# Kernel optimization log

Measured on AMD Instinct MI355X. Metric: run time of the kernel, lower is better.

The kernel has to match this reference:

```python
import jax, jax.numpy as jnp
import numpy as np
from jax import lax

B, C, H, W = 32, 256, 56, 56
K = 3  # kernel_size

def setup_inputs() -> dict:
    key = jax.random.key(0)
    k1, k2, k3 = jax.random.split(key, 3)
    x = jax.random.normal(k1, (B, C, H, W), dtype=jnp.float32)
    # 1x1 conv weight Conv2d(C, C*K*K, 1) flattened to a linear map [C*K*K, C]
    Wk = jax.random.normal(k2, (C * K * K, C), dtype=jnp.float32) * 0.02
    bk = jax.random.normal(k3, (C * K * K,), dtype=jnp.float32) * 0.02
    return {"x": x, "Wk": Wk, "bk": bk}

def reference(x, Wk, bk):
    b, c, h, w = x.shape
    # kernel generator: global avg pool -> 1x1 conv -> relu
    pooled = x.mean(axis=(2, 3))                       # [B, C]
    kern = jax.nn.relu(pooled @ Wk.T + bk)             # [B, C*K*K]
    kern = kern.reshape(b * c, 1, K, K)                # OIHW, one filter per (b,c)
    # per-sample, per-channel depthwise conv: groups = B*C
    xr = x.reshape(1, b * c, h, w)
    out = lax.conv_general_dilated(
        xr, kern,
        window_strides=(1, 1),
        padding=[(K // 2, K // 2), (K // 2, K // 2)],
        feature_group_count=b * c,
        dimension_numbers=("NCHW", "OIHW", "NCHW"),
    )
    return out.reshape(b, c, h, w)
```

## Files before the change

kernel.cpp:

```cpp
#include <hip/hip_runtime.h>

#define B_  32
#define C_  256
#define H_  56
#define W_  56
#define HW  3136
#define KK  9
#define OC  2304
#define NPLANES (B_*C_)

typedef float v4f __attribute__((ext_vector_type(4)));

__global__ __launch_bounds__(256) void pool_kernel(const float* __restrict__ x,
                                                   float* __restrict__ pooled) {
    const int wid  = threadIdx.x >> 6;
    const int lane = threadIdx.x & 63;
    const int plane = blockIdx.x * 4 + wid;
    const float4* xp = (const float4*)(x + (size_t)plane * HW);

    float s = 0.f;
    #pragma unroll
    for (int k = 0; k < 12; ++k) {
        float4 v = xp[lane + k * 64];
        s += (v.x + v.y) + (v.z + v.w);
    }
    if (lane < 16) {
        float4 v = xp[768 + lane];
        s += (v.x + v.y) + (v.z + v.w);
    }
    #pragma unroll
    for (int off = 32; off > 0; off >>= 1)
        s += __shfl_down(s, off, 64);
    if (lane == 0)
        pooled[plane] = s * (1.0f / (float)HW);
}

__global__ __launch_bounds__(256) void dconv_kernel(const float* __restrict__ x,
                                                    const float* __restrict__ pooled,
                                                    const float* __restrict__ Wk,
                                                    const float* __restrict__ bk,
                                                    float* __restrict__ out) {
    const int plane = blockIdx.x;
    const int b = plane >> 8;
    const int c = plane & 255;
    __shared__ float lds[58 * 58];
    __shared__ float wsh[KK];
    const int t = threadIdx.x;

    const float4* xp = (const float4*)(x + (size_t)plane * HW);
    float4 v0 = xp[t];
    float4 v1 = xp[t + 256];
    float4 v2 = xp[t + 512];
    float4 v3 = make_float4(0.f, 0.f, 0.f, 0.f);
    if (t < 16) v3 = xp[t + 768];

    if (t < 144) {
        const int o  = t >> 4;
        const int ch = (t & 15) << 4;
        const int og = c * KK + o;
        const float4* wr = (const float4*)(Wk + (size_t)og * C_ + ch);
        const float4* pr = (const float4*)(pooled + b * C_ + ch);
        float s = 0.f;
        #pragma unroll
        for (int i = 0; i < 4; ++i) {
            float4 w = wr[i];
            float4 p = pr[i];
            s += w.x * p.x + w.y * p.y + w.z * p.z + w.w * p.w;
        }
        #pragma unroll
        for (int off = 8; off > 0; off >>= 1)
            s += __shfl_down(s, off, 16);
        if ((t & 15) == 0)
            wsh[o] = fmaxf(s + bk[og], 0.f);
    }

    if (t < 58) { lds[t] = 0.f; lds[57 * 58 + t] = 0.f; }
    if (t < 56) { lds[(t + 1) * 58] = 0.f; lds[(t + 1) * 58 + 57] = 0.f; }

    {
        int s, r, c0, base;
        s = t;        r = s / 14; c0 = (s % 14) * 4; base = (r + 1) * 58 + c0 + 1;
        lds[base] = v0.x; lds[base + 1] = v0.y; lds[base + 2] = v0.z; lds[base + 3] = v0.w;
        s = t + 256;  r = s / 14; c0 = (s % 14) * 4; base = (r + 1) * 58 + c0 + 1;
        lds[base] = v1.x; lds[base + 1] = v1.y; lds[base + 2] = v1.z; lds[base + 3] = v1.w;
        s = t + 512;  r = s / 14; c0 = (s % 14) * 4; base = (r + 1) * 58 + c0 + 1;
        lds[base] = v2.x; lds[base + 1] = v2.y; lds[base + 2] = v2.z; lds[base + 3] = v2.w;
        if (t < 16) {
            s = t + 768; r = s / 14; c0 = (s % 14) * 4; base = (r + 1) * 58 + c0 + 1;
            lds[base] = v3.x; lds[base + 1] = v3.y; lds[base + 2] = v3.z; lds[base + 3] = v3.w;
        }
    }

    __syncthreads();

    const float w0 = wsh[0], w1 = wsh[1], w2 = wsh[2],
                w3 = wsh[3], w4 = wsh[4], w5 = wsh[5],
                w6 = wsh[6], w7 = wsh[7], w8 = wsh[8];

    float* op = out + (size_t)plane * HW;

    for (int i = t; i < 392; i += 256) {
        const int rp = i / 14;
        const int c0 = (i % 14) * 4;
        const float* R0 = &lds[(2 * rp + 0) * 58 + c0];
        const float* R1 = &lds[(2 * rp + 1) * 58 + c0];
        const float* R2 = &lds[(2 * rp + 2) * 58 + c0];
        const float* R3 = &lds[(2 * rp + 3) * 58 + c0];
        float2 p0 = *(const float2*)(R0), p1 = *(const float2*)(R0 + 2), p2 = *(const float2*)(R0 + 4);
        float2 q0 = *(const float2*)(R1), q1 = *(const float2*)(R1 + 2), q2 = *(const float2*)(R1 + 4);
        float2 r0 = *(const float2*)(R2), r1 = *(const float2*)(R2 + 2), r2 = *(const float2*)(R2 + 4);
        float2 s0 = *(const float2*)(R3), s1 = *(const float2*)(R3 + 2), s2 = *(const float2*)(R3 + 4);
        const float a0 = p0.x, a1 = p0.y, a2 = p1.x, a3 = p1.y, a4 = p2.x, a5 = p2.y;
        const float b0 = q0.x, b1 = q0.y, b2 = q1.x, b3 = q1.y, b4 = q2.x, b5 = q2.y;
        const float c0f = r0.x, c1f = r0.y, c2f = r1.x, c3f = r1.y, c4f = r2.x, c5f = r2.y;
        const float d0 = s0.x, d1 = s0.y, d2 = s1.x, d3 = s1.y, d4 = s2.x, d5 = s2.y;

        v4f t0, t1;
        t0.x = a0*w0 + a1*w1 + a2*w2 + b0*w3 + b1*w4 + b2*w5 + c0f*w6 + c1f*w7 + c2f*w8;
        t0.y = a1*w0 + a2*w1 + a3*w2 + b1*w3 + b2*w4 + b3*w5 + c1f*w6 + c2f*w7 + c3f*w8;
        t0.z = a2*w0 + a3*w1 + a4*w2 + b2*w3 + b3*w4 + b4*w5 + c2f*w6 + c3f*w7 + c4f*w8;
        t0.w = a3*w0 + a4*w1 + a5*w2 + b3*w3 + b4*w4 + b5*w5 + c3f*w6 + c4f*w7 + c5f*w8;
        t1.x = b0*w0 + b1*w1 + b2*w2 + c0f*w3 + c1f*w4 + c2f*w5 + d0*w6 + d1*w7 + d2*w8;
        t1.y = b1*w0 + b2*w1 + b3*w2 + c1f*w3 + c2f*w4 + c3f*w5 + d1*w6 + d2*w7 + d3*w8;
        t1.z = b2*w0 + b3*w1 + b4*w2 + c2f*w3 + c3f*w4 + c4f*w5 + d2*w6 + d3*w7 + d4*w8;
        t1.w = b3*w0 + b4*w1 + b5*w2 + c3f*w3 + c4f*w4 + c5f*w5 + d3*w6 + d4*w7 + d5*w8;

        __builtin_nontemporal_store(t0, (v4f*)(op + (2 * rp + 0) * W_ + c0));
        __builtin_nontemporal_store(t1, (v4f*)(op + (2 * rp + 1) * W_ + c0));
    }
}

extern "C" void kernel_launch(void* const* d_in, const int* in_sizes, int n_in,
                              void* d_out, int out_size, void* d_ws, size_t ws_size,
                              hipStream_t stream) {
    const float* x  = (const float*)d_in[0];
    const float* Wk = (const float*)d_in[1];
    const float* bk = (const float*)d_in[2];
    float* out = (float*)d_out;

    float* pooled = (float*)d_ws;

    pool_kernel<<<NPLANES / 4, 256, 0, stream>>>(x, pooled);
    dconv_kernel<<<NPLANES, 256, 0, stream>>>(x, pooled, Wk, bk, out);
}
```

Measured before the change: 198.9 us.

## Process eight planes per block with double-buffered LDS staging and coalesced stores

The depthwise conv kernel becomes persistent-style: each block walks eight consecutive planes. While it computes the current plane, it prefetches the next plane and its generated filter into registers and a second LDS buffer. Output is staged through an LDS tile, so global stores are fully contiguous float4 writes. This aims to hide global load latency and cut per-block launch overhead, but it uses much more LDS per block (about 39KB) and adds an extra barrier per plane, which lowers occupancy and parallelism (1024 blocks instead of 8192).

```diff
diff --git a/kernel.cpp b/kernel.cpp
--- a/kernel.cpp
+++ b/kernel.cpp
@@ -6,8 +6,9 @@
 #define W_  56
 #define HW  3136
 #define KK  9
-#define OC  2304
 #define NPLANES (B_*C_)
+#define NP  8
+#define DGRID (NPLANES/NP)
 
 typedef float v4f __attribute__((ext_vector_type(4)));
 
@@ -35,26 +36,14 @@
         pooled[plane] = s * (1.0f / (float)HW);
 }
 
-__global__ __launch_bounds__(256) void dconv_kernel(const float* __restrict__ x,
-                                                    const float* __restrict__ pooled,
-                                                    const float* __restrict__ Wk,
-                                                    const float* __restrict__ bk,
-                                                    float* __restrict__ out) {
-    const int plane = blockIdx.x;
-    const int b = plane >> 8;
-    const int c = plane & 255;
-    __shared__ float lds[58 * 58];
-    __shared__ float wsh[KK];
-    const int t = threadIdx.x;
-
-    const float4* xp = (const float4*)(x + (size_t)plane * HW);
-    float4 v0 = xp[t];
-    float4 v1 = xp[t + 256];
-    float4 v2 = xp[t + 512];
-    float4 v3 = make_float4(0.f, 0.f, 0.f, 0.f);
-    if (t < 16) v3 = xp[t + 768];
-
+__device__ __forceinline__ void kerngen(int t, int plane,
+                                        const float* __restrict__ pooled,
+                                        const float* __restrict__ Wk,
+                                        const float* __restrict__ bk,
+                                        float* __restrict__ wdst) {
     if (t < 144) {
+        const int b  = plane >> 8;
+        const int c  = plane & 255;
         const int o  = t >> 4;
         const int ch = (t & 15) << 4;
         const int og = c * KK + o;
@@ -71,62 +60,115 @@
         for (int off = 8; off > 0; off >>= 1)
             s += __shfl_down(s, off, 16);
         if ((t & 15) == 0)
-            wsh[o] = fmaxf(s + bk[og], 0.f);
+            wdst[o] = fmaxf(s + bk[og], 0.f);
+    }
+}
+
+__device__ __forceinline__ void stage_write(float* __restrict__ dst, int t,
+                                            float4 v0, float4 v1, float4 v2, float4 v3) {
+    int s, r, c0, base;
+    s = t;        r = s / 14; c0 = (s % 14) * 4; base = (r + 1) * 58 + c0 + 1;
+    dst[base] = v0.x; dst[base + 1] = v0.y; dst[base + 2] = v0.z; dst[base + 3] = v0.w;
+    s = t + 256;  r = s / 14; c0 = (s % 14) * 4; base = (r + 1) * 58 + c0 + 1;
+    dst[base] = v1.x; dst[base + 1] = v1.y; dst[base + 2] = v1.z; dst[base + 3] = v1.w;
+    s = t + 512;  r = s / 14; c0 = (s % 14) * 4; base = (r + 1) * 58 + c0 + 1;
+    dst[base] = v2.x; dst[base + 1] = v2.y; dst[base + 2] = v2.z; dst[base + 3] = v2.w;
+    if (t < 16) {
+        s = t + 768; r = s / 14; c0 = (s % 14) * 4; base = (r + 1) * 58 + c0 + 1;
+        dst[base] = v3.x; dst[base + 1] = v3.y; dst[base + 2] = v3.z; dst[base + 3] = v3.w;
+    }
+}
+
+__global__ __launch_bounds__(256, 4) void dconv_kernel(const float* __restrict__ x,
+                                                       const float* __restrict__ pooled,
+                                                       const float* __restrict__ Wk,
+                                                       const float* __restrict__ bk,
+                                                       float* __restrict__ out) {
+    __shared__ float buf[2][58 * 58];
+    __shared__ float ost[56 * 56];
+    __shared__ float wsh[2][16];
+
+    const int t  = threadIdx.x;
+    const int p0 = blockIdx.x * NP;
+
+    #pragma unroll
+    for (int q = 0; q < 2; ++q) {
+        if (t < 58) { buf[q][t] = 0.f; buf[q][57 * 58 + t] = 0.f; }
+        if (t < 56) { buf[q][(t + 1) * 58] = 0.f; buf[q][(t + 1) * 58 + 57] = 0.f; }
     }
 
-    if (t < 58) { lds[t] = 0.f; lds[57 * 58 + t] = 0.f; }
-    if (t < 56) { lds[(t + 1) * 58] = 0.f; lds[(t + 1) * 58 + 57] = 0.f; }
-
+    float4 s0, s1, s2, s3 = make_float4(0.f, 0.f, 0.f, 0.f);
     {
-        int s, r, c0, base;
-        s = t;        r = s / 14; c0 = (s % 14) * 4; base = (r + 1) * 58 + c0 + 1;
-        lds[base] = v0.x; lds[base + 1] = v0.y; lds[base + 2] = v0.z; lds[base + 3] = v0.w;
-        s = t + 256;  r = s / 14; c0 = (s % 14) * 4; base = (r + 1) * 58 + c0 + 1;
-        lds[base] = v1.x; lds[base + 1] = v1.y; lds[base + 2] = v1.z; lds[base + 3] = v1.w;
-        s = t + 512;  r = s / 14; c0 = (s % 14) * 4; base = (r + 1) * 58 + c0 + 1;
-        lds[base] = v2.x; lds[base + 1] = v2.y; lds[base + 2] = v2.z; lds[base + 3] = v2.w;
-        if (t < 16) {
-            s = t + 768; r = s / 14; c0 = (s % 14) * 4; base = (r + 1) * 58 + c0 + 1;
-            lds[base] = v3.x; lds[base + 1] = v3.y; lds[base + 2] = v3.z; lds[base + 3] = v3.w;
-        }
+        const float4* xp = (const float4*)(x + (size_t)p0 * HW);
+        s0 = xp[t]; s1 = xp[t + 256]; s2 = xp[t + 512];
+        if (t < 16) s3 = xp[t + 768];
     }
-
+    kerngen(t, p0, pooled, Wk, bk, wsh[0]);
+    stage_write(buf[0], t, s0, s1, s2, s3);
     __syncthreads();
 
-    const float w0 = wsh[0], w1 = wsh[1], w2 = wsh[2],
-                w3 = wsh[3], w4 = wsh[4], w5 = wsh[5],
-                w6 = wsh[6], w7 = wsh[7], w8 = wsh[8];
+    for (int p = 0; p < NP; ++p) {
+        const int cur = p & 1, nxt = cur ^ 1;
+        const bool more = (p + 1 < NP);
 
-    float* op = out + (size_t)plane * HW;
+        if (more) {
+            const float4* xp = (const float4*)(x + (size_t)(p0 + p + 1) * HW);
+            s0 = xp[t]; s1 = xp[t + 256]; s2 = xp[t + 512];
+            if (t < 16) s3 = xp[t + 768];
+            kerngen(t, p0 + p + 1, pooled, Wk, bk, wsh[nxt]);
+        }
 
-    for (int i = t; i < 392; i += 256) {
-        const int rp = i / 14;
-        const int c0 = (i % 14) * 4;
-        const float* R0 = &lds[(2 * rp + 0) * 58 + c0];
-        const float* R1 = &lds[(2 * rp + 1) * 58 + c0];
-        const float* R2 = &lds[(2 * rp + 2) * 58 + c0];
-        const float* R3 = &lds[(2 * rp + 3) * 58 + c0];
-        float2 p0 = *(const float2*)(R0), p1 = *(const float2*)(R0 + 2), p2 = *(const float2*)(R0 + 4);
-        float2 q0 = *(const float2*)(R1), q1 = *(const float2*)(R1 + 2), q2 = *(const float2*)(R1 + 4);
-        float2 r0 = *(const float2*)(R2), r1 = *(const float2*)(R2 + 2), r2 = *(const float2*)(R2 + 4);
-        float2 s0 = *(const float2*)(R3), s1 = *(const float2*)(R3 + 2), s2 = *(const float2*)(R3 + 4);
-        const float a0 = p0.x, a1 = p0.y, a2 = p1.x, a3 = p1.y, a4 = p2.x, a5 = p2.y;
-        const float b0 = q0.x, b1 = q0.y, b2 = q1.x, b3 = q1.y, b4 = q2.x, b5 = q2.y;
-        const float c0f = r0.x, c1f = r0.y, c2f = r1.x, c3f = r1.y, c4f = r2.x, c5f = r2.y;
-        const float d0 = s0.x, d1 = s0.y, d2 = s1.x, d3 = s1.y, d4 = s2.x, d5 = s2.y;
+        {
+            const float* wc = wsh[cur];
+            const float w0 = wc[0], w1 = wc[1], w2 = wc[2],
+                        w3 = wc[3], w4 = wc[4], w5 = wc[5],
+                        w6 = wc[6], w7 = wc[7], w8 = wc[8];
+            const float* bs = buf[cur];
+            for (int i = t; i < 392; i += 256) {
+                const int rp = i / 14;
+                const int c0 = (i % 14) * 4;
+                const float* R0 = &bs[(2 * rp + 0) * 58 + c0];
+                const float* R1 = &bs[(2 * rp + 1) * 58 + c0];
+                const float* R2 = &bs[(2 * rp + 2) * 58 + c0];
+                const float* R3 = &bs[(2 * rp + 3) * 58 + c0];
+                float2 p0v = *(const float2*)(R0), p1v = *(const float2*)(R0 + 2), p2v = *(const float2*)(R0 + 4);
+                float2 q0v = *(const float2*)(R1), q1v = *(const float2*)(R1 + 2), q2v = *(const float2*)(R1 + 4);
+                float2 r0v = *(const float2*)(R2), r1v = *(const float2*)(R2 + 2), r2v = *(const float2*)(R2 + 4);
+                float2 u0v = *(const float2*)(R3), u1v = *(const float2*)(R3 + 2), u2v = *(const float2*)(R3 + 4);
+                const float a0 = p0v.x, a1 = p0v.y, a2 = p1v.x, a3 = p1v.y, a4 = p2v.x, a5 = p2v.y;
+                const float b0 = q0v.x, b1 = q0v.y, b2 = q1v.x, b3 = q1v.y, b4 = q2v.x, b5 = q2v.y;
+                const float e0 = r0v.x, e1 = r0v.y, e2 = r1v.x, e3 = r1v.y, e4 = r2v.x, e5 = r2v.y;
+                const float d0 = u0v.x, d1 = u0v.y, d2 = u1v.x, d3 = u1v.y, d4 = u2v.x, d5 = u2v.y;
 
-        v4f t0, t1;
-        t0.x = a0*w0 + a1*w1 + a2*w2 + b0*w3 + b1*w4 + b2*w5 + c0f*w6 + c1f*w7 + c2f*w8;
-        t0.y = a1*w0 + a2*w1 + a3*w2 + b1*w3 + b2*w4 + b3*w5 + c1f*w6 + c2f*w7 + c3f*w8;
-        t0.z = a2*w0 + a3*w1 + a4*w2 + b2*w3 + b3*w4 + b4*w5 + c2f*w6 + c3f*w7 + c4f*w8;
-        t0.w = a3*w0 + a4*w1 + a5*w2 + b3*w3 + b4*w4 + b5*w5 + c3f*w6 + c4f*w7 + c5f*w8;
-        t1.x = b0*w0 + b1*w1 + b2*w2 + c0f*w3 + c1f*w4 + c2f*w5 + d0*w6 + d1*w7 + d2*w8;
-        t1.y = b1*w0 + b2*w1 + b3*w2 + c1f*w3 + c2f*w4 + c3f*w5 + d1*w6 + d2*w7 + d3*w8;
-        t1.z = b2*w0 + b3*w1 + b4*w2 + c2f*w3 + c3f*w4 + c4f*w5 + d2*w6 + d3*w7 + d4*w8;
-        t1.w = b3*w0 + b4*w1 + b5*w2 + c3f*w3 + c4f*w4 + c5f*w5 + d3*w6 + d4*w7 + d5*w8;
+                v4f t0, t1;
+                t0.x = a0*w0 + a1*w1 + a2*w2 + b0*w3 + b1*w4 + b2*w5 + e0*w6 + e1*w7 + e2*w8;
+                t0.y = a1*w0 + a2*w1 + a3*w2 + b1*w3 + b2*w4 + b3*w5 + e1*w6 + e2*w7 + e3*w8;
+                t0.z = a2*w0 + a3*w1 + a4*w2 + b2*w3 + b3*w4 + b4*w5 + e2*w6 + e3*w7 + e4*w8;
+                t0.w = a3*w0 + a4*w1 + a5*w2 + b3*w3 + b4*w4 + b5*w5 + e3*w6 + e4*w7 + e5*w8;
+                t1.x = b0*w0 + b1*w1 + b2*w2 + e0*w3 + e1*w4 + e2*w5 + d0*w6 + d1*w7 + d2*w8;
+                t1.y = b1*w0 + b2*w1 + b3*w2 + e1*w3 + e2*w4 + e3*w5 + d1*w6 + d2*w7 + d3*w8;
+                t1.z = b2*w0 + b3*w1 + b4*w2 + e2*w3 + e3*w4 + e4*w5 + d2*w6 + d3*w7 + d4*w8;
+                t1.w = b3*w0 + b4*w1 + b5*w2 + e3*w3 + e4*w4 + e5*w5 + d3*w6 + d4*w7 + d5*w8;
 
-        __builtin_nontemporal_store(t0, (v4f*)(op + (2 * rp + 0) * W_ + c0));
-        __builtin_nontemporal_store(t1, (v4f*)(op + (2 * rp + 1) * W_ + c0));
+                *(v4f*)&ost[(2 * rp + 0) * 56 + c0] = t0;
+                *(v4f*)&ost[(2 * rp + 1) * 56 + c0] = t1;
+            }
+        }
+        __syncthreads();
+
+        {
+            float* op = out + (size_t)(p0 + p) * HW;
+            const v4f* os = (const v4f*)ost;
+            __builtin_nontemporal_store(os[t],       (v4f*)op + t);
+            __builtin_nontemporal_store(os[t + 256], (v4f*)op + t + 256);
+            __builtin_nontemporal_store(os[t + 512], (v4f*)op + t + 512);
+            if (t < 16)
+                __builtin_nontemporal_store(os[t + 768], (v4f*)op + t + 768);
+        }
+
+        if (more)
+            stage_write(buf[nxt], t, s0, s1, s2, s3);
+        __syncthreads();
     }
 }
 
@@ -141,5 +183,5 @@
     float* pooled = (float*)d_ws;
 
     pool_kernel<<<NPLANES / 4, 256, 0, stream>>>(x, pooled);
-    dconv_kernel<<<NPLANES, 256, 0, stream>>>(x, pooled, Wk, bk, out);
+    dconv_kernel<<<DGRID, 256, 0, stream>>>(x, pooled, Wk, bk, out);
 }
```

Measured after the change: 206.4 us. 3.8% more time.

## Drop LDS halo tile in depthwise conv, read neighbours directly from global/cache

Applied to the files above, without the earlier changes.

The padded 58x58 shared-memory tile and its staging stores are removed. Each thread now loads its four input rows straight from global memory, using float4 loads plus scalar left and right halo loads, and handles the zero padding with predicates. Launch bounds add a minimum-blocks hint of 8 to raise occupancy now that LDS use is minimal. The trade is more redundant global and L1/L2 traffic from overlapping halo reads and unaligned scalar loads, in exchange for removing the LDS round trip.

```diff
diff --git a/kernel.cpp b/kernel.cpp
--- a/kernel.cpp
+++ b/kernel.cpp
@@ -6,7 +6,6 @@
 #define W_  56
 #define HW  3136
 #define KK  9
-#define OC  2304
 #define NPLANES (B_*C_)
 
 typedef float v4f __attribute__((ext_vector_type(4)));
@@ -35,24 +34,16 @@
         pooled[plane] = s * (1.0f / (float)HW);
 }
 
-__global__ __launch_bounds__(256) void dconv_kernel(const float* __restrict__ x,
-                                                    const float* __restrict__ pooled,
-                                                    const float* __restrict__ Wk,
-                                                    const float* __restrict__ bk,
-                                                    float* __restrict__ out) {
+__global__ __launch_bounds__(256, 8) void dconv_kernel(const float* __restrict__ x,
+                                                       const float* __restrict__ pooled,
+                                                       const float* __restrict__ Wk,
+                                                       const float* __restrict__ bk,
+                                                       float* __restrict__ out) {
     const int plane = blockIdx.x;
     const int b = plane >> 8;
     const int c = plane & 255;
-    __shared__ float lds[58 * 58];
     __shared__ float wsh[KK];
     const int t = threadIdx.x;
-
-    const float4* xp = (const float4*)(x + (size_t)plane * HW);
-    float4 v0 = xp[t];
-    float4 v1 = xp[t + 256];
-    float4 v2 = xp[t + 512];
-    float4 v3 = make_float4(0.f, 0.f, 0.f, 0.f);
-    if (t < 16) v3 = xp[t + 768];
 
     if (t < 144) {
         const int o  = t >> 4;
@@ -73,58 +64,80 @@
         if ((t & 15) == 0)
             wsh[o] = fmaxf(s + bk[og], 0.f);
     }
-
-    if (t < 58) { lds[t] = 0.f; lds[57 * 58 + t] = 0.f; }
-    if (t < 56) { lds[(t + 1) * 58] = 0.f; lds[(t + 1) * 58 + 57] = 0.f; }
-
-    {
-        int s, r, c0, base;
-        s = t;        r = s / 14; c0 = (s % 14) * 4; base = (r + 1) * 58 + c0 + 1;
-        lds[base] = v0.x; lds[base + 1] = v0.y; lds[base + 2] = v0.z; lds[base + 3] = v0.w;
-        s = t + 256;  r = s / 14; c0 = (s % 14) * 4; base = (r + 1) * 58 + c0 + 1;
-        lds[base] = v1.x; lds[base + 1] = v1.y; lds[base + 2] = v1.z; lds[base + 3] = v1.w;
-        s = t + 512;  r = s / 14; c0 = (s % 14) * 4; base = (r + 1) * 58 + c0 + 1;
-        lds[base] = v2.x; lds[base + 1] = v2.y; lds[base + 2] = v2.z; lds[base + 3] = v2.w;
-        if (t < 16) {
-            s = t + 768; r = s / 14; c0 = (s % 14) * 4; base = (r + 1) * 58 + c0 + 1;
-            lds[base] = v3.x; lds[base + 1] = v3.y; lds[base + 2] = v3.z; lds[base + 3] = v3.w;
-        }
-    }
-
     __syncthreads();
 
     const float w0 = wsh[0], w1 = wsh[1], w2 = wsh[2],
                 w3 = wsh[3], w4 = wsh[4], w5 = wsh[5],
                 w6 = wsh[6], w7 = wsh[7], w8 = wsh[8];
 
+    const float* xp = x + (size_t)plane * HW;
     float* op = out + (size_t)plane * HW;
 
     for (int i = t; i < 392; i += 256) {
         const int rp = i / 14;
         const int c0 = (i % 14) * 4;
-        const float* R0 = &lds[(2 * rp + 0) * 58 + c0];
-        const float* R1 = &lds[(2 * rp + 1) * 58 + c0];
-        const float* R2 = &lds[(2 * rp + 2) * 58 + c0];
-        const float* R3 = &lds[(2 * rp + 3) * 58 + c0];
-        float2 p0 = *(const float2*)(R0), p1 = *(const float2*)(R0 + 2), p2 = *(const float2*)(R0 + 4);
-        float2 q0 = *(const float2*)(R1), q1 = *(const float2*)(R1 + 2), q2 = *(const float2*)(R1 + 4);
-        float2 r0 = *(const float2*)(R2), r1 = *(const float2*)(R2 + 2), r2 = *(const float2*)(R2 + 4);
-        float2 s0 = *(const float2*)(R3), s1 = *(const float2*)(R3 + 2), s2 = *(const float2*)(R3 + 4);
-        const float a0 = p0.x, a1 = p0.y, a2 = p1.x, a3 = p1.y, a4 = p2.x, a5 = p2.y;
-        const float b0 = q0.x, b1 = q0.y, b2 = q1.x, b3 = q1.y, b4 = q2.x, b5 = q2.y;
-        const float c0f = r0.x, c1f = r0.y, c2f = r1.x, c3f = r1.y, c4f = r2.x, c5f = r2.y;
-        const float d0 = s0.x, d1 = s0.y, d2 = s1.x, d3 = s1.y, d4 = s2.x, d5 = s2.y;
+        const bool cl = (c0 > 0);
+        const bool cr = (c0 < 52);
+
+        float a00 = 0.f, a01 = 0.f, a02 = 0.f, a03 = 0.f;
+        float a10 = 0.f, a11 = 0.f, a12 = 0.f, a13 = 0.f;
+
+        {
+            const int r = 2 * rp - 1;
+            const float* rw = xp + (r < 0 ? 0 : r) * W_;
+            float4 m = *(const float4*)(rw + c0);
+            float vl = cl ? rw[c0 - 1] : 0.f;
+            float vr = cr ? rw[c0 + 4] : 0.f;
+            if (r < 0) { m.x = 0.f; m.y = 0.f; m.z = 0.f; m.w = 0.f; vl = 0.f; vr = 0.f; }
+            a00 += w0 * vl  + w1 * m.x + w2 * m.y;
+            a01 += w0 * m.x + w1 * m.y + w2 * m.z;
+            a02 += w0 * m.y + w1 * m.z + w2 * m.w;
+            a03 += w0 * m.z + w1 * m.w + w2 * vr;
+        }
+        {
+            const float* rw = xp + (2 * rp) * W_;
+            float4 m = *(const float4*)(rw + c0);
+            float vl = cl ? rw[c0 - 1] : 0.f;
+            float vr = cr ? rw[c0 + 4] : 0.f;
+            a00 += w3 * vl  + w4 * m.x + w5 * m.y;
+            a01 += w3 * m.x + w4 * m.y + w5 * m.z;
+            a02 += w3 * m.y + w4 * m.z + w5 * m.w;
+            a03 += w3 * m.z + w4 * m.w + w5 * vr;
+            a10 += w0 * vl  + w1 * m.x + w2 * m.y;
+            a11 += w0 * m.x + w1 * m.y + w2 * m.z;
+            a12 += w0 * m.y + w1 * m.z + w2 * m.w;
+            a13 += w0 * m.z + w1 * m.w + w2 * vr;
+        }
+        {
+            const float* rw = xp + (2 * rp + 1) * W_;
+            float4 m = *(const float4*)(rw + c0);
+            float vl = cl ? rw[c0 - 1] : 0.f;
+            float vr = cr ? rw[c0 + 4] : 0.f;
+            a00 += w6 * vl  + w7 * m.x + w8 * m.y;
+            a01 += w6 * m.x + w7 * m.y + w8 * m.z;
+            a02 += w6 * m.y + w7 * m.z + w8 * m.w;
+            a03 += w6 * m.z + w7 * m.w + w8 * vr;
+            a10 += w3 * vl  + w4 * m.x + w5 * m.y;
+            a11 += w3 * m.x + w4 * m.y + w5 * m.z;
+            a12 += w3 * m.y + w4 * m.z + w5 * m.w;
+            a13 += w3 * m.z + w4 * m.w + w5 * vr;
+        }
+        {
+            const int r = 2 * rp + 2;
+            const float* rw = xp + (r > 55 ? 55 : r) * W_;
+            float4 m = *(const float4*)(rw + c0);
+            float vl = cl ? rw[c0 - 1] : 0.f;
+            float vr = cr ? rw[c0 + 4] : 0.f;
+            if (r > 55) { m.x = 0.f; m.y = 0.f; m.z = 0.f; m.w = 0.f; vl = 0.f; vr = 0.f; }
+            a10 += w6 * vl  + w7 * m.x + w8 * m.y;
+            a11 += w6 * m.x + w7 * m.y + w8 * m.z;
+            a12 += w6 * m.y + w7 * m.z + w8 * m.w;
+            a13 += w6 * m.z + w7 * m.w + w8 * vr;
+        }
 
         v4f t0, t1;
-        t0.x = a0*w0 + a1*w1 + a2*w2 + b0*w3 + b1*w4 + b2*w5 + c0f*w6 + c1f*w7 + c2f*w8;
-        t0.y = a1*w0 + a2*w1 + a3*w2 + b1*w3 + b2*w4 + b3*w5 + c1f*w6 + c2f*w7 + c3f*w8;
-        t0.z = a2*w0 + a3*w1 + a4*w2 + b2*w3 + b3*w4 + b4*w5 + c2f*w6 + c3f*w7 + c4f*w8;
-        t0.w = a3*w0 + a4*w1 + a5*w2 + b3*w3 + b4*w4 + b5*w5 + c3f*w6 + c4f*w7 + c5f*w8;
-        t1.x = b0*w0 + b1*w1 + b2*w2 + c0f*w3 + c1f*w4 + c2f*w5 + d0*w6 + d1*w7 + d2*w8;
-        t1.y = b1*w0 + b2*w1 + b3*w2 + c1f*w3 + c2f*w4 + c3f*w5 + d1*w6 + d2*w7 + d3*w8;
-        t1.z = b2*w0 + b3*w1 + b4*w2 + c2f*w3 + c3f*w4 + c4f*w5 + d2*w6 + d3*w7 + d4*w8;
-        t1.w = b3*w0 + b4*w1 + b5*w2 + c3f*w3 + c4f*w4 + c5f*w5 + d3*w6 + d4*w7 + d5*w8;
-
+        t0.x = a00; t0.y = a01; t0.z = a02; t0.w = a03;
+        t1.x = a10; t1.y = a11; t1.z = a12; t1.w = a13;
         __builtin_nontemporal_store(t0, (v4f*)(op + (2 * rp + 0) * W_ + c0));
         __builtin_nontemporal_store(t1, (v4f*)(op + (2 * rp + 1) * W_ + c0));
     }
```

Result: slower. 221.2 us (+11.2%).

## Replace LDS halo staging in depthwise conv with direct global loads and lane shuffles

Applied to the files above, without the earlier changes.

The depthwise conv kernel no longer stages the padded 58x58 plane in shared memory. Each thread now loads four row segments of four floats straight from global memory and gets left and right halo values from neighbouring lanes with width-16 shuffles, masking image borders to zero. This removes the shared-memory fill, its index arithmetic and most of the LDS footprint, and the launch bounds now ask for higher occupancy. In exchange, adjacent row pairs re-read overlapping rows, which relies on the caches. Two of every sixteen lanes sit idle, and the output stores are now ordinary stores instead of nontemporal ones.

```diff
diff --git a/kernel.cpp b/kernel.cpp
--- a/kernel.cpp
+++ b/kernel.cpp
@@ -6,7 +6,6 @@
 #define W_  56
 #define HW  3136
 #define KK  9
-#define OC  2304
 #define NPLANES (B_*C_)
 
 typedef float v4f __attribute__((ext_vector_type(4)));
@@ -35,24 +34,16 @@
         pooled[plane] = s * (1.0f / (float)HW);
 }
 
-__global__ __launch_bounds__(256) void dconv_kernel(const float* __restrict__ x,
-                                                    const float* __restrict__ pooled,
-                                                    const float* __restrict__ Wk,
-                                                    const float* __restrict__ bk,
-                                                    float* __restrict__ out) {
+__global__ __launch_bounds__(256, 8) void dconv_kernel(const float* __restrict__ x,
+                                                       const float* __restrict__ pooled,
+                                                       const float* __restrict__ Wk,
+                                                       const float* __restrict__ bk,
+                                                       float* __restrict__ out) {
     const int plane = blockIdx.x;
     const int b = plane >> 8;
     const int c = plane & 255;
-    __shared__ float lds[58 * 58];
     __shared__ float wsh[KK];
     const int t = threadIdx.x;
-
-    const float4* xp = (const float4*)(x + (size_t)plane * HW);
-    float4 v0 = xp[t];
-    float4 v1 = xp[t + 256];
-    float4 v2 = xp[t + 512];
-    float4 v3 = make_float4(0.f, 0.f, 0.f, 0.f);
-    if (t < 16) v3 = xp[t + 768];
 
     if (t < 144) {
         const int o  = t >> 4;
@@ -73,60 +64,62 @@
         if ((t & 15) == 0)
             wsh[o] = fmaxf(s + bk[og], 0.f);
     }
-
-    if (t < 58) { lds[t] = 0.f; lds[57 * 58 + t] = 0.f; }
-    if (t < 56) { lds[(t + 1) * 58] = 0.f; lds[(t + 1) * 58 + 57] = 0.f; }
-
-    {
-        int s, r, c0, base;
-        s = t;        r = s / 14; c0 = (s % 14) * 4; base = (r + 1) * 58 + c0 + 1;
-        lds[base] = v0.x; lds[base + 1] = v0.y; lds[base + 2] = v0.z; lds[base + 3] = v0.w;
-        s = t + 256;  r = s / 14; c0 = (s % 14) * 4; base = (r + 1) * 58 + c0 + 1;
-        lds[base] = v1.x; lds[base + 1] = v1.y; lds[base + 2] = v1.z; lds[base + 3] = v1.w;
-        s = t + 512;  r = s / 14; c0 = (s % 14) * 4; base = (r + 1) * 58 + c0 + 1;
-        lds[base] = v2.x; lds[base + 1] = v2.y; lds[base + 2] = v2.z; lds[base + 3] = v2.w;
-        if (t < 16) {
-            s = t + 768; r = s / 14; c0 = (s % 14) * 4; base = (r + 1) * 58 + c0 + 1;
-            lds[base] = v3.x; lds[base + 1] = v3.y; lds[base + 2] = v3.z; lds[base + 3] = v3.w;
-        }
-    }
-
     __syncthreads();
 
     const float w0 = wsh[0], w1 = wsh[1], w2 = wsh[2],
                 w3 = wsh[3], w4 = wsh[4], w5 = wsh[5],
                 w6 = wsh[6], w7 = wsh[7], w8 = wsh[8];
 
+    const float* xp = x + (size_t)plane * HW;
     float* op = out + (size_t)plane * HW;
 
-    for (int i = t; i < 392; i += 256) {
-        const int rp = i / 14;
-        const int c0 = (i % 14) * 4;
-        const float* R0 = &lds[(2 * rp + 0) * 58 + c0];
-        const float* R1 = &lds[(2 * rp + 1) * 58 + c0];
-        const float* R2 = &lds[(2 * rp + 2) * 58 + c0];
-        const float* R3 = &lds[(2 * rp + 3) * 58 + c0];
-        float2 p0 = *(const float2*)(R0), p1 = *(const float2*)(R0 + 2), p2 = *(const float2*)(R0 + 4);
-        float2 q0 = *(const float2*)(R1), q1 = *(const float2*)(R1 + 2), q2 = *(const float2*)(R1 + 4);
-        float2 r0 = *(const float2*)(R2), r1 = *(const float2*)(R2 + 2), r2 = *(const float2*)(R2 + 4);
-        float2 s0 = *(const float2*)(R3), s1 = *(const float2*)(R3 + 2), s2 = *(const float2*)(R3 + 4);
-        const float a0 = p0.x, a1 = p0.y, a2 = p1.x, a3 = p1.y, a4 = p2.x, a5 = p2.y;
-        const float b0 = q0.x, b1 = q0.y, b2 = q1.x, b3 = q1.y, b4 = q2.x, b5 = q2.y;
-        const float c0f = r0.x, c1f = r0.y, c2f = r1.x, c3f = r1.y, c4f = r2.x, c5f = r2.y;
-        const float d0 = s0.x, d1 = s0.y, d2 = s1.x, d3 = s1.y, d4 = s2.x, d5 = s2.y;
+    const int lane = t & 63;
+    const int k    = lane & 15;
+    const int g    = lane >> 4;
+    const int wv   = t >> 6;
+    const bool ka  = (k < 14);
+    const int c0   = ka ? (k << 2) : 0;
+    const bool hl  = (k > 0);
+    const bool hr  = (k < 13);
 
-        v4f t0, t1;
-        t0.x = a0*w0 + a1*w1 + a2*w2 + b0*w3 + b1*w4 + b2*w5 + c0f*w6 + c1f*w7 + c2f*w8;
-        t0.y = a1*w0 + a2*w1 + a3*w2 + b1*w3 + b2*w4 + b3*w5 + c1f*w6 + c2f*w7 + c3f*w8;
-        t0.z = a2*w0 + a3*w1 + a4*w2 + b2*w3 + b3*w4 + b4*w5 + c2f*w6 + c3f*w7 + c4f*w8;
-        t0.w = a3*w0 + a4*w1 + a5*w2 + b3*w3 + b4*w4 + b5*w5 + c3f*w6 + c4f*w7 + c5f*w8;
-        t1.x = b0*w0 + b1*w1 + b2*w2 + c0f*w3 + c1f*w4 + c2f*w5 + d0*w6 + d1*w7 + d2*w8;
-        t1.y = b1*w0 + b2*w1 + b3*w2 + c1f*w3 + c2f*w4 + c3f*w5 + d1*w6 + d2*w7 + d3*w8;
-        t1.z = b2*w0 + b3*w1 + b4*w2 + c2f*w3 + c3f*w4 + c4f*w5 + d2*w6 + d3*w7 + d4*w8;
-        t1.w = b3*w0 + b4*w1 + b5*w2 + c3f*w3 + c4f*w4 + c5f*w5 + d3*w6 + d4*w7 + d5*w8;
+    #pragma unroll
+    for (int half = 0; half < 2; ++half) {
+        const int rp = half * 16 + wv * 4 + g;
+        if (rp >= 28) break;
 
-        __builtin_nontemporal_store(t0, (v4f*)(op + (2 * rp + 0) * W_ + c0));
-        __builtin_nontemporal_store(t1, (v4f*)(op + (2 * rp + 1) * W_ + c0));
+        const int rA = (rp == 0)  ? 0  : 2 * rp - 1;
+        const int rB = (rp == 27) ? 55 : 2 * rp + 2;
+
+        float4 A  = *(const float4*)(xp + rA * W_ + c0);
+        float4 M  = *(const float4*)(xp + (2 * rp) * W_ + c0);
+        float4 N  = *(const float4*)(xp + (2 * rp + 1) * W_ + c0);
+        float4 Bv = *(const float4*)(xp + rB * W_ + c0);
+        if (rp == 0)  { A.x = 0.f;  A.y = 0.f;  A.z = 0.f;  A.w = 0.f; }
+        if (rp == 27) { Bv.x = 0.f; Bv.y = 0.f; Bv.z = 0.f; Bv.w = 0.f; }
+
+        if (ka) {
+            float Al = __shfl_up(A.w, 1, 16),  Ar = __shfl_down(A.x, 1, 16);
+            float Ml = __shfl_up(M.w, 1, 16),  Mr = __shfl_down(M.x, 1, 16);
+            float Nl = __shfl_up(N.w, 1, 16),  Nr = __shfl_down(N.x, 1, 16);
+            float Bl = __shfl_up(Bv.w, 1, 16), Br = __shfl_down(Bv.x, 1, 16);
+            Al = hl ? Al : 0.f;  Ml = hl ? Ml : 0.f;
+            Nl = hl ? Nl : 0.f;  Bl = hl ? Bl : 0.f;
+            Ar = hr ? Ar : 0.f;  Mr = hr ? Mr : 0.f;
+            Nr = hr ? Nr : 0.f;  Br = hr ? Br : 0.f;
+
+            v4f t0, t1;
+            t0.x = w0*Al  + w1*A.x  + w2*A.y  + w3*Ml  + w4*M.x  + w5*M.y  + w6*Nl  + w7*N.x  + w8*N.y;
+            t0.y = w0*A.x + w1*A.y  + w2*A.z  + w3*M.x + w4*M.y  + w5*M.z  + w6*N.x + w7*N.y  + w8*N.z;
+            t0.z = w0*A.y + w1*A.z  + w2*A.w  + w3*M.y + w4*M.z  + w5*M.w  + w6*N.y + w7*N.z  + w8*N.w;
+            t0.w = w0*A.z + w1*A.w  + w2*Ar   + w3*M.z + w4*M.w  + w5*Mr   + w6*N.z + w7*N.w  + w8*Nr;
+            t1.x = w0*Ml  + w1*M.x  + w2*M.y  + w3*Nl  + w4*N.x  + w5*N.y  + w6*Bl  + w7*Bv.x + w8*Bv.y;
+            t1.y = w0*M.x + w1*M.y  + w2*M.z  + w3*N.x + w4*N.y  + w5*N.z  + w6*Bv.x+ w7*Bv.y + w8*Bv.z;
+            t1.z = w0*M.y + w1*M.z  + w2*M.w  + w3*N.y + w4*N.z  + w5*N.w  + w6*Bv.y+ w7*Bv.z + w8*Bv.w;
+            t1.w = w0*M.z + w1*M.w  + w2*Mr   + w3*N.z + w4*N.w  + w5*Nr   + w6*Bv.z+ w7*Bv.w + w8*Br;
+
+            *(v4f*)(op + (2 * rp + 0) * W_ + c0) = t0;
+            *(v4f*)(op + (2 * rp + 1) * W_ + c0) = t1;
+        }
     }
 }
 
```

Result: no change. 198.5 us (-0.2%).
